# Optimization experiments

Measured on AMD Instinct MI355X. Metric: run time of the kernel, lower is better.

The kernel has to match this reference:

```python
import jax, jax.numpy as jnp
import numpy as np

B, S, D, H, HD = 1, 4096, 1024, 16, 64
HALF = HD // 2


def setup_inputs() -> dict:
    key = jax.random.key(0)
    ks = jax.random.split(key, 8)
    std = 0.02
    x = jax.random.normal(ks[0], (B, S, D), dtype=jnp.float32)
    wq_w = jax.random.normal(ks[1], (D, D), dtype=jnp.float32) * std
    wk_w = jax.random.normal(ks[2], (D, D), dtype=jnp.float32) * std
    wv_w = jax.random.normal(ks[3], (D, D), dtype=jnp.float32) * std
    wo_w = jax.random.normal(ks[4], (D, D), dtype=jnp.float32) * std
    wq_b = jnp.zeros((D,), jnp.float32)
    wk_b = jnp.zeros((D,), jnp.float32)
    wv_b = jnp.zeros((D,), jnp.float32)
    wo_b = jnp.zeros((D,), jnp.float32)
    # LLaMA-style rotary frequencies: theta = 10000^{-2i/HD}
    inv_freq = 1.0 / (10000.0 ** (jnp.arange(0, HD, 2, dtype=jnp.float32) / HD))  # [HALF]
    t = jnp.arange(S, dtype=jnp.float32)
    angles = jnp.outer(t, inv_freq)  # [S, HALF]
    freqs_cos = jnp.cos(angles)
    freqs_sin = jnp.sin(angles)
    # causal additive mask (finite large-negative to stay grad-safe)
    mask = jnp.triu(jnp.full((S, S), -1e9, dtype=jnp.float32), k=1)[None, None]
    return {
        "x": x, "start_pos": 0, "freqs_cos": freqs_cos, "freqs_sin": freqs_sin,
        "mask": mask,
        "wq_w": wq_w, "wq_b": wq_b, "wk_w": wk_w, "wk_b": wk_b,
        "wv_w": wv_w, "wv_b": wv_b, "wo_w": wo_w, "wo_b": wo_b,
    }


def _apply_rope(t, cos, sin):
    # t: [B, S, H, HD]; cos/sin: [S, HALF]. Complex multiply on consecutive pairs.
    b, s, h, hd = t.shape
    t2 = t.reshape(b, s, h, hd // 2, 2)
    x0, x1 = t2[..., 0], t2[..., 1]
    c = cos[None, :, None, :]
    sn = sin[None, :, None, :]
    o0 = x0 * c - x1 * sn
    o1 = x0 * sn + x1 * c
    return jnp.stack([o0, o1], axis=-1).reshape(b, s, h, hd)


def reference(x, start_pos, freqs_cos, freqs_sin, mask,
              wq_w, wq_b, wk_w, wk_b, wv_w, wv_b, wo_w, wo_b):
    bsz, seqlen, dim = x.shape
    q = (x @ wq_w.T + wq_b).reshape(bsz, seqlen, H, HD)
    k = (x @ wk_w.T + wk_b).reshape(bsz, seqlen, H, HD)
    v = (x @ wv_w.T + wv_b).reshape(bsz, seqlen, H, HD)
    q = _apply_rope(q, freqs_cos, freqs_sin)
    k = _apply_rope(k, freqs_cos, freqs_sin)
    # [B, H, S, HD]
    q = q.transpose(0, 2, 1, 3)
    k = k.transpose(0, 2, 1, 3)
    v = v.transpose(0, 2, 1, 3)
    scores = jnp.einsum('bhqd,bhkd->bhqk', q, k) / jnp.sqrt(jnp.float32(HD))
    scores = scores + mask
    probs = jax.nn.softmax(scores.astype(jnp.float32), axis=-1).astype(q.dtype)
    out = jnp.einsum('bhqk,bhkd->bhqd', probs, v)  # [B, H, S, HD]
    out = out.transpose(0, 2, 1, 3).reshape(bsz, seqlen, dim)
    return out @ wo_w.T + wo_b
```

## Files before the change

### kernel.cpp

```cpp
#include <hip/hip_runtime.h>


#define S_LEN 4096
#define DIM   1024
#define NH    16
#define HD    64

typedef __attribute__((ext_vector_type(8))) short bf16x8;
typedef __attribute__((ext_vector_type(4))) float f32x4;

__device__ __forceinline__ unsigned short f2b(float f) {
  union { float f; unsigned int u; } v; v.f = f;
  unsigned int r = (v.u + 0x7fffu + ((v.u >> 16) & 1u)) >> 16;
  return (unsigned short)r;
}
__device__ __forceinline__ float b2f(unsigned short h) {
  union { unsigned int u; float f; } v; v.u = ((unsigned int)h) << 16;
  return v.f;
}
__device__ __forceinline__ unsigned int pk2t(float a, float b) {
  union { float f; unsigned int u; } x, y; x.f = a; y.f = b;
  return (x.u >> 16) | (y.u & 0xffff0000u);
}
__device__ __forceinline__ void gload16(const void* g, void* l) {
  __builtin_amdgcn_global_load_lds(
      (const __attribute__((address_space(1))) unsigned int*)g,
      (__attribute__((address_space(3))) unsigned int*)l, 16, 0, 0);
}
__device__ __forceinline__ f32x4 fzero4() { f32x4 z = {0.f, 0.f, 0.f, 0.f}; return z; }

__global__ void cvt_all(const float* __restrict__ x, const float* __restrict__ wq,
                        const float* __restrict__ wk, const float* __restrict__ wv,
                        const float* __restrict__ wo, const float* __restrict__ qb,
                        const float* __restrict__ kb, const float* __restrict__ vbs,
                        const float* __restrict__ ob, unsigned short* __restrict__ xb,
                        unsigned short* __restrict__ wqkvb, unsigned short* __restrict__ wobb,
                        float* __restrict__ biasq, float* __restrict__ biaso) {
  int i = blockIdx.x * 256 + threadIdx.x;
  if (i < 2097152) {
    const float* src; unsigned short* dst; int off;
    if (i < 1048576)      { src = x;  dst = xb;              off = i; }
    else if (i < 1310720) { src = wq; dst = wqkvb;           off = i - 1048576; }
    else if (i < 1572864) { src = wk; dst = wqkvb + 1048576; off = i - 1310720; }
    else if (i < 1835008) { src = wv; dst = wqkvb + 2097152; off = i - 1572864; }
    else                  { src = wo; dst = wobb;            off = i - 1835008; }
    float4 v = ((const float4*)src)[off];
    unsigned int lo = (unsigned int)f2b(v.x) | ((unsigned int)f2b(v.y) << 16);
    unsigned int hi = (unsigned int)f2b(v.z) | ((unsigned int)f2b(v.w) << 16);
    ((uint2*)dst)[off] = make_uint2(lo, hi);
  } else if (i < 2097152 + 1024) {
    int j = i - 2097152;
    if (j < 256)      ((float4*)biasq)[j]              = ((const float4*)qb)[j];
    else if (j < 512) ((float4*)(biasq + 1024))[j-256] = ((const float4*)kb)[j-256];
    else if (j < 768) ((float4*)(biasq + 2048))[j-512] = ((const float4*)vbs)[j-512];
    else              ((float4*)biaso)[j-768]          = ((const float4*)ob)[j-768];
  }
}

__global__ __launch_bounds__(256) void gemm_qkv(
    const unsigned short* __restrict__ A, const unsigned short* __restrict__ B,
    const float* __restrict__ bias, unsigned short* __restrict__ dq,
    unsigned short* __restrict__ dk, unsigned short* __restrict__ vtout,
    const float* __restrict__ fc, const float* __restrict__ fs, int K) {
  __shared__ alignas(16) unsigned short sA[2][128 * 32];
  __shared__ alignas(16) unsigned short sB[2][128 * 32];
  const int tid = threadIdx.x;
  const int lane = tid & 63, wave = tid >> 6;
  const int ln = lane & 15, quad = lane >> 4;
  const int bm = blockIdx.x * 128, bn = blockIdx.y * 128;
  const int wr = (wave >> 1) * 64, wc = (wave & 1) * 64;

  f32x4 acc[4][4];
#pragma unroll
  for (int i = 0; i < 4; ++i)
#pragma unroll
    for (int j = 0; j < 4; ++j) acc[i][j] = fzero4();

#pragma unroll
  for (int i = 0; i < 2; ++i) {
    int o = (i * 256 + tid) * 16;
    int e = o >> 1;
    int row = e >> 5, col = e & 31;
    gload16(A + (size_t)(bm + row) * K + col, (char*)sA[0] + o);
    gload16(B + (size_t)(bn + row) * K + col, (char*)sB[0] + o);
  }

  int buf = 0;
  for (int k0 = 0; k0 < K; k0 += 32, buf ^= 1) {
    __syncthreads();
    if (k0 + 32 < K) {
#pragma unroll
      for (int i = 0; i < 2; ++i) {
        int o = (i * 256 + tid) * 16;
        int e = o >> 1;
        int row = e >> 5, col = e & 31;
        gload16(A + (size_t)(bm + row) * K + k0 + 32 + col, (char*)sA[buf ^ 1] + o);
        gload16(B + (size_t)(bn + row) * K + k0 + 32 + col, (char*)sB[buf ^ 1] + o);
      }
    }
    bf16x8 af[4], bfr[4];
#pragma unroll
    for (int i = 0; i < 4; ++i) {
      af[i]  = *(const bf16x8*)&sA[buf][(wr + i * 16 + ln) * 32 + quad * 8];
      bfr[i] = *(const bf16x8*)&sB[buf][(wc + i * 16 + ln) * 32 + quad * 8];
    }
#pragma unroll
    for (int i = 0; i < 4; ++i)
#pragma unroll
      for (int j = 0; j < 4; ++j)
        acc[i][j] = __builtin_amdgcn_mfma_f32_16x16x32_bf16(af[i], bfr[j], acc[i][j], 0, 0, 0);
  }

  const int bufi = bn >> 10;
  const int hq = ((bn & 1023) + wc) >> 6;
  if (bufi < 2) {
    unsigned short* const base = bufi == 0 ? dq : dk;
    const float qsc = bufi == 0 ? 0.180336880f : 1.0f;
#pragma unroll
    for (int i = 0; i < 4; ++i)
#pragma unroll
      for (int j = 0; j < 4; ++j) {
        int n = bn + wc + j * 16 + ln;
        float bi = bias[n];
        int hd = j * 16 + ln;
        int pi = hd >> 1;
        bool evn = (ln & 1) == 0;
#pragma unroll
        for (int r = 0; r < 4; ++r) {
          int m = bm + wr + i * 16 + quad * 4 + r;
          float val = acc[i][j][r] + bi;
          float par = __shfl_xor(val, 1);
          float c = fc[m * 32 + pi], sn = fs[m * 32 + pi];
          float o = evn ? (val * c - par * sn) : (par * sn + val * c);
          base[((size_t)(hq * S_LEN + m)) * HD + hd] = f2b(o * qsc);
        }
      }
  } else {
    __syncthreads();
    unsigned short* scr =
        (wave < 2 ? (unsigned short*)sA : (unsigned short*)sB) + (wave & 1) * 4096;
#pragma unroll
    for (int i = 0; i < 4; ++i)
#pragma unroll
      for (int j = 0; j < 4; ++j) {
        int n = bn + wc + j * 16 + ln;
        float bi = bias[n];
        int hd = j * 16 + ln;
#pragma unroll
        for (int r = 0; r < 4; ++r) {
          int sl = i * 16 + quad * 4 + r;
          int byte = hd * 128 + ((((sl >> 3) ^ (hd & 7)) << 4)) + (sl & 7) * 2;
          *(unsigned short*)((char*)scr + byte) = f2b(acc[i][j][r] + bi);
        }
      }
#pragma unroll
    for (int pass = 0; pass < 4; ++pass) {
      int row = pass * 16 + ln;
      uint4 d0 = *(uint4*)((char*)scr + row * 128 + (((quad * 2) ^ (row & 7)) << 4));
      uint4 d1 = *(uint4*)((char*)scr + row * 128 + (((quad * 2 + 1) ^ (row & 7)) << 4));
      uint4* dst = (uint4*)(vtout + ((size_t)(hq * HD + row)) * S_LEN + bm + wr + quad * 16);
      dst[0] = d0;
      dst[1] = d1;
    }
  }
}

__global__ __launch_bounds__(256) void gemm_out(
    const unsigned short* __restrict__ A, const unsigned short* __restrict__ B,
    const float* __restrict__ bias, float* __restrict__ outF, int N, int K) {
  __shared__ alignas(16) unsigned short sA[2][128 * 32];
  __shared__ alignas(16) unsigned short sB[2][64 * 32];
  const int tid = threadIdx.x;
  const int lane = tid & 63, wave = tid >> 6;
  const int ln = lane & 15, quad = lane >> 4;
  const int bm = blockIdx.x * 128, bn = blockIdx.y * 64;
  const int wr = (wave >> 1) * 64, wc = (wave & 1) * 32;

  f32x4 acc[4][2];
#pragma unroll
  for (int i = 0; i < 4; ++i)
#pragma unroll
    for (int j = 0; j < 2; ++j) acc[i][j] = fzero4();

  {
#pragma unroll
    for (int i = 0; i < 2; ++i) {
      int o = (i * 256 + tid) * 16;
      int e = o >> 1;
      int row = e >> 5, col = e & 31;
      gload16(A + (size_t)(bm + row) * K + col, (char*)sA[0] + o);
    }
    int o = tid * 16;
    int e = o >> 1;
    int row = e >> 5, col = e & 31;
    gload16(B + (size_t)(bn + row) * K + col, (char*)sB[0] + o);
  }

  int buf = 0;
  for (int k0 = 0; k0 < K; k0 += 32, buf ^= 1) {
    __syncthreads();
    if (k0 + 32 < K) {
#pragma unroll
      for (int i = 0; i < 2; ++i) {
        int o = (i * 256 + tid) * 16;
        int e = o >> 1;
        int row = e >> 5, col = e & 31;
        gload16(A + (size_t)(bm + row) * K + k0 + 32 + col, (char*)sA[buf ^ 1] + o);
      }
      int o = tid * 16;
      int e = o >> 1;
      int row = e >> 5, col = e & 31;
      gload16(B + (size_t)(bn + row) * K + k0 + 32 + col, (char*)sB[buf ^ 1] + o);
    }
    bf16x8 af[4], bfr[2];
#pragma unroll
    for (int i = 0; i < 4; ++i)
      af[i] = *(const bf16x8*)&sA[buf][(wr + i * 16 + ln) * 32 + quad * 8];
#pragma unroll
    for (int j = 0; j < 2; ++j)
      bfr[j] = *(const bf16x8*)&sB[buf][(wc + j * 16 + ln) * 32 + quad * 8];
#pragma unroll
    for (int i = 0; i < 4; ++i)
#pragma unroll
      for (int j = 0; j < 2; ++j)
        acc[i][j] = __builtin_amdgcn_mfma_f32_16x16x32_bf16(af[i], bfr[j], acc[i][j], 0, 0, 0);
  }

#pragma unroll
  for (int i = 0; i < 4; ++i)
#pragma unroll
    for (int j = 0; j < 2; ++j) {
      int n = bn + wc + j * 16 + ln;
      float bi = bias[n];
#pragma unroll
      for (int r = 0; r < 4; ++r) {
        int m = bm + wr + i * 16 + quad * 4 + r;
        outF[(size_t)m * N + n] = acc[i][j][r] + bi;
      }
    }
}

__device__ __forceinline__ bf16x8 lds_swzK(const unsigned short* s, int row, int chunk) {
  int byte = row * 128 + ((chunk ^ ((row >> 2) & 7)) << 4);
  return *(const bf16x8*)((const char*)s + byte);
}
__device__ __forceinline__ bf16x8 lds_swzV(const unsigned short* s, int row, int chunk) {
  int byte = row * 128 + ((chunk ^ (row & 7)) << 4);
  return *(const bf16x8*)((const char*)s + byte);
}

__global__ __launch_bounds__(256, 4) void flash_kernel(
    const unsigned short* __restrict__ qg, const unsigned short* __restrict__ kg,
    const unsigned short* __restrict__ vtg, unsigned short* __restrict__ attn) {
  __shared__ alignas(16) unsigned short sK[2][64 * 64];
  __shared__ alignas(16) unsigned short sV[2][64 * 64];
  __shared__ alignas(16) unsigned short sP[4 * 16 * 72];

  const int tid = threadIdx.x;
  const int lane = tid & 63, wave = tid >> 6;
  const int ln = lane & 15, quad = lane >> 4;
  const int c = blockIdx.x;
  const int h = 2 * (c & 7) + ((c >> 3) & 1);
  const int xp = c >> 4;

  const unsigned short* qh = qg + (size_t)h * (S_LEN * HD);
  const unsigned short* kh = kg + (size_t)h * (S_LEN * HD);
  const unsigned short* vh = vtg + (size_t)h * (HD * S_LEN);

  bf16x8 ones;
#pragma unroll
  for (int j = 0; j < 8; ++j) ones[j] = (short)0x3F80;
  unsigned short* pw = &sP[wave * (16 * 72)];

  for (int p = 0; p < 2; ++p) {
    const int qb = p == 0 ? xp : 63 - xp;
    const int q0 = qb * 64;
    const int qrow = q0 + wave * 16;

    bf16x8 qf[2];
    qf[0] = *(const bf16x8*)(qh + (size_t)(qrow + ln) * HD + quad * 8);
    qf[1] = *(const bf16x8*)(qh + (size_t)(qrow + ln) * HD + 32 + quad * 8);

    f32x4 o_acc[4];
    f32x4 l_acc = fzero4();
#pragma unroll
    for (int t = 0; t < 4; ++t) o_acc[t] = fzero4();

    const int nkv = qb + 1;

    __syncthreads();
#pragma unroll
    for (int i = 0; i < 2; ++i) {
      int ob = (i * 256 + tid) * 16;
      int row = ob >> 7;
      int ch = (ob >> 4) & 7;
      gload16(kh + (size_t)row * HD + ((ch ^ ((row >> 2) & 7)) << 3), (char*)sK[0] + ob);
      gload16(vh + (size_t)row * S_LEN + ((ch ^ (row & 7)) << 3), (char*)sV[0] + ob);
    }

    int buf = 0;
    for (int kt = 0; kt < nkv; ++kt, buf ^= 1) {
      const int kv0 = kt * 64;
      __syncthreads();
      if (kt + 1 < nkv) {
        const int kv1 = kv0 + 64;
#pragma unroll
        for (int i = 0; i < 2; ++i) {
          int ob = (i * 256 + tid) * 16;
          int row = ob >> 7;
          int ch = (ob >> 4) & 7;
          gload16(kh + (size_t)(kv1 + row) * HD + ((ch ^ ((row >> 2) & 7)) << 3),
                  (char*)sK[buf ^ 1] + ob);
          gload16(vh + (size_t)row * S_LEN + kv1 + ((ch ^ (row & 7)) << 3),
                  (char*)sV[buf ^ 1] + ob);
        }
      }

      const unsigned short* kp = sK[buf];
      const unsigned short* vp = sV[buf];
      f32x4 sc[4];
#pragma unroll
      for (int t = 0; t < 4; ++t) sc[t] = fzero4();
#pragma unroll
      for (int t = 0; t < 4; ++t) {
        int krow = ln * 4 + t;
        bf16x8 kb0 = lds_swzK(kp, krow, quad);
        bf16x8 kb1 = lds_swzK(kp, krow, 4 + quad);
        sc[t] = __builtin_amdgcn_mfma_f32_16x16x32_bf16(qf[0], kb0, sc[t], 0, 0, 0);
        sc[t] = __builtin_amdgcn_mfma_f32_16x16x32_bf16(qf[1], kb1, sc[t], 0, 0, 0);
      }

      if (kt == nkv - 1) {
#pragma unroll
        for (int r = 0; r < 4; ++r) {
          int row = qrow + quad * 4 + r;
          int colb = kv0 + ln * 4;
          float p0 = (colb + 0 <= row) ? __builtin_amdgcn_exp2f(sc[0][r]) : 0.0f;
          float p1 = (colb + 1 <= row) ? __builtin_amdgcn_exp2f(sc[1][r]) : 0.0f;
          float p2 = (colb + 2 <= row) ? __builtin_amdgcn_exp2f(sc[2][r]) : 0.0f;
          float p3 = (colb + 3 <= row) ? __builtin_amdgcn_exp2f(sc[3][r]) : 0.0f;
          *(uint2*)&pw[(quad * 4 + r) * 72 + ln * 4] = make_uint2(pk2t(p0, p1), pk2t(p2, p3));
        }
      } else {
#pragma unroll
        for (int r = 0; r < 4; ++r) {
          float p0 = __builtin_amdgcn_exp2f(sc[0][r]);
          float p1 = __builtin_amdgcn_exp2f(sc[1][r]);
          float p2 = __builtin_amdgcn_exp2f(sc[2][r]);
          float p3 = __builtin_amdgcn_exp2f(sc[3][r]);
          *(uint2*)&pw[(quad * 4 + r) * 72 + ln * 4] = make_uint2(pk2t(p0, p1), pk2t(p2, p3));
        }
      }

      bf16x8 pa0 = *(const bf16x8*)&pw[ln * 72 + quad * 8];
      bf16x8 pa1 = *(const bf16x8*)&pw[ln * 72 + 32 + quad * 8];

      l_acc = __builtin_amdgcn_mfma_f32_16x16x32_bf16(pa0, ones, l_acc, 0, 0, 0);
      l_acc = __builtin_amdgcn_mfma_f32_16x16x32_bf16(pa1, ones, l_acc, 0, 0, 0);

#pragma unroll
      for (int t = 0; t < 4; ++t) {
        int vrow = t * 16 + ln;
        bf16x8 vb0 = lds_swzV(vp, vrow, quad);
        bf16x8 vb1 = lds_swzV(vp, vrow, 4 + quad);
        o_acc[t] = __builtin_amdgcn_mfma_f32_16x16x32_bf16(pa0, vb0, o_acc[t], 0, 0, 0);
        o_acc[t] = __builtin_amdgcn_mfma_f32_16x16x32_bf16(pa1, vb1, o_acc[t], 0, 0, 0);
      }
    }

    float inv[4];
#pragma unroll
    for (int r = 0; r < 4; ++r) inv[r] = 1.0f / l_acc[r];
#pragma unroll
    for (int t = 0; t < 4; ++t)
#pragma unroll
      for (int r = 0; r < 4; ++r) {
        int row = qrow + quad * 4 + r;
        attn[(size_t)row * DIM + h * HD + t * 16 + ln] = f2b(o_acc[t][r] * inv[r]);
      }
  }
}

extern "C" void kernel_launch(void* const* d_in, const int* in_sizes, int n_in,
                              void* d_out, int out_size, void* d_ws, size_t ws_size,
                              hipStream_t stream) {
  const float* x    = (const float*)d_in[0];
  const float* fc   = (const float*)d_in[2];
  const float* fs   = (const float*)d_in[3];
  const float* wqw  = (const float*)d_in[5];
  const float* wqb  = (const float*)d_in[6];
  const float* wkw  = (const float*)d_in[7];
  const float* wkb  = (const float*)d_in[8];
  const float* wvw  = (const float*)d_in[9];
  const float* wvb  = (const float*)d_in[10];
  const float* wow  = (const float*)d_in[11];
  const float* wobf = (const float*)d_in[12];
  float* out = (float*)d_out;

  char* ws = (char*)d_ws;
  const size_t MB = (size_t)1 << 20;
  unsigned short* xb    = (unsigned short*)(ws + 0);
  unsigned short* wqkvb = (unsigned short*)(ws + 8 * MB);
  unsigned short* wobb  = (unsigned short*)(ws + 16 * MB);
  float* biasq = (float*)(ws + 18 * MB);
  float* biaso = (float*)(ws + 18 * MB + 65536);
  unsigned short* qb_ = (unsigned short*)(ws + 19 * MB);
  unsigned short* kb_ = (unsigned short*)(ws + 27 * MB);
  unsigned short* vt  = (unsigned short*)(ws + 35 * MB);
  unsigned short* attn = (unsigned short*)(ws + 0);

  cvt_all<<<8196, 256, 0, stream>>>(x, wqw, wkw, wvw, wow, wqb, wkb, wvb, wobf,
                                    xb, wqkvb, wobb, biasq, biaso);
  gemm_qkv<<<dim3(32, 24), 256, 0, stream>>>(xb, wqkvb, biasq, qb_, kb_, vt, fc, fs, 1024);
  flash_kernel<<<512, 256, 0, stream>>>(qb_, kb_, vt, attn);
  gemm_out<<<dim3(32, 16), 256, 0, stream>>>(attn, wobb, biaso, out, 1024, 1024);
}
```

Before: 267.7 us.

## Process paired causal query tiles concurrently in one 512-thread block sharing K/V loads

Each block now runs 8 waves, split into two groups that handle a short and a long causal query tile at the same time, instead of processing the two tiles one after the other. The groups share the double-buffered K/V tiles in LDS, which halves K/V global loads for the pair. The group whose tile is already complete skips compute via a continue but still takes part in loads and barriers. Block ordering is also remapped so heavier pairs are scheduled first. The cost is idle waves in the short-tile group during the tail of the loop.

```diff
diff --git a/kernel.cpp b/kernel.cpp
--- a/kernel.cpp
+++ b/kernel.cpp
@@ -249,136 +249,122 @@
   return *(const bf16x8*)((const char*)s + byte);
 }
 
-__global__ __launch_bounds__(256, 4) void flash_kernel(
+__global__ __launch_bounds__(512, 2) void flash_kernel(
     const unsigned short* __restrict__ qg, const unsigned short* __restrict__ kg,
     const unsigned short* __restrict__ vtg, unsigned short* __restrict__ attn) {
   __shared__ alignas(16) unsigned short sK[2][64 * 64];
   __shared__ alignas(16) unsigned short sV[2][64 * 64];
-  __shared__ alignas(16) unsigned short sP[4 * 16 * 72];
+  __shared__ alignas(16) unsigned short sP[8 * 16 * 72];
 
   const int tid = threadIdx.x;
   const int lane = tid & 63, wave = tid >> 6;
+  const int w = wave & 3, grp = wave >> 2;
   const int ln = lane & 15, quad = lane >> 4;
   const int c = blockIdx.x;
   const int h = 2 * (c & 7) + ((c >> 3) & 1);
-  const int xp = c >> 4;
+  const int u = c >> 4;
+  const int a = (u < 16) ? u : 47 - u;
+  const int q0 = (grp == 0 ? a : 63 - a) * 64;
+  const int qrow = q0 + w * 16;
 
   const unsigned short* qh = qg + (size_t)h * (S_LEN * HD);
   const unsigned short* kh = kg + (size_t)h * (S_LEN * HD);
   const unsigned short* vh = vtg + (size_t)h * (HD * S_LEN);
 
+  bf16x8 qf[2];
+  qf[0] = *(const bf16x8*)(qh + (size_t)(qrow + ln) * HD + quad * 8);
+  qf[1] = *(const bf16x8*)(qh + (size_t)(qrow + ln) * HD + 32 + quad * 8);
+
+  f32x4 o_acc[4];
+  f32x4 l_acc = fzero4();
+#pragma unroll
+  for (int t = 0; t < 4; ++t) o_acc[t] = fzero4();
   bf16x8 ones;
 #pragma unroll
   for (int j = 0; j < 8; ++j) ones[j] = (short)0x3F80;
   unsigned short* pw = &sP[wave * (16 * 72)];
 
-  for (int p = 0; p < 2; ++p) {
-    const int qb = p == 0 ? xp : 63 - xp;
-    const int q0 = qb * 64;
-    const int qrow = q0 + wave * 16;
-
-    bf16x8 qf[2];
-    qf[0] = *(const bf16x8*)(qh + (size_t)(qrow + ln) * HD + quad * 8);
-    qf[1] = *(const bf16x8*)(qh + (size_t)(qrow + ln) * HD + 32 + quad * 8);
-
-    f32x4 o_acc[4];
-    f32x4 l_acc = fzero4();
-#pragma unroll
-    for (int t = 0; t < 4; ++t) o_acc[t] = fzero4();
-
-    const int nkv = qb + 1;
-
+  const int nkv = 64 - a;
+  const int srow = tid >> 3, sch = tid & 7;
+
+  gload16(kh + (size_t)srow * HD + ((sch ^ ((srow >> 2) & 7)) << 3), (char*)sK[0] + tid * 16);
+  gload16(vh + (size_t)srow * S_LEN + ((sch ^ (srow & 7)) << 3), (char*)sV[0] + tid * 16);
+
+  int buf = 0;
+  for (int kt = 0; kt < nkv; ++kt, buf ^= 1) {
+    const int kv0 = kt * 64;
     __syncthreads();
-#pragma unroll
-    for (int i = 0; i < 2; ++i) {
-      int ob = (i * 256 + tid) * 16;
-      int row = ob >> 7;
-      int ch = (ob >> 4) & 7;
-      gload16(kh + (size_t)row * HD + ((ch ^ ((row >> 2) & 7)) << 3), (char*)sK[0] + ob);
-      gload16(vh + (size_t)row * S_LEN + ((ch ^ (row & 7)) << 3), (char*)sV[0] + ob);
-    }
-
-    int buf = 0;
-    for (int kt = 0; kt < nkv; ++kt, buf ^= 1) {
-      const int kv0 = kt * 64;
-      __syncthreads();
-      if (kt + 1 < nkv) {
-        const int kv1 = kv0 + 64;
-#pragma unroll
-        for (int i = 0; i < 2; ++i) {
-          int ob = (i * 256 + tid) * 16;
-          int row = ob >> 7;
-          int ch = (ob >> 4) & 7;
-          gload16(kh + (size_t)(kv1 + row) * HD + ((ch ^ ((row >> 2) & 7)) << 3),
-                  (char*)sK[buf ^ 1] + ob);
-          gload16(vh + (size_t)row * S_LEN + kv1 + ((ch ^ (row & 7)) << 3),
-                  (char*)sV[buf ^ 1] + ob);
-        }
-      }
-
-      const unsigned short* kp = sK[buf];
-      const unsigned short* vp = sV[buf];
-      f32x4 sc[4];
-#pragma unroll
-      for (int t = 0; t < 4; ++t) sc[t] = fzero4();
-#pragma unroll
-      for (int t = 0; t < 4; ++t) {
-        int krow = ln * 4 + t;
-        bf16x8 kb0 = lds_swzK(kp, krow, quad);
-        bf16x8 kb1 = lds_swzK(kp, krow, 4 + quad);
-        sc[t] = __builtin_amdgcn_mfma_f32_16x16x32_bf16(qf[0], kb0, sc[t], 0, 0, 0);
-        sc[t] = __builtin_amdgcn_mfma_f32_16x16x32_bf16(qf[1], kb1, sc[t], 0, 0, 0);
-      }
-
-      if (kt == nkv - 1) {
-#pragma unroll
-        for (int r = 0; r < 4; ++r) {
-          int row = qrow + quad * 4 + r;
-          int colb = kv0 + ln * 4;
-          float p0 = (colb + 0 <= row) ? __builtin_amdgcn_exp2f(sc[0][r]) : 0.0f;
-          float p1 = (colb + 1 <= row) ? __builtin_amdgcn_exp2f(sc[1][r]) : 0.0f;
-          float p2 = (colb + 2 <= row) ? __builtin_amdgcn_exp2f(sc[2][r]) : 0.0f;
-          float p3 = (colb + 3 <= row) ? __builtin_amdgcn_exp2f(sc[3][r]) : 0.0f;
-          *(uint2*)&pw[(quad * 4 + r) * 72 + ln * 4] = make_uint2(pk2t(p0, p1), pk2t(p2, p3));
-        }
-      } else {
-#pragma unroll
-        for (int r = 0; r < 4; ++r) {
-          float p0 = __builtin_amdgcn_exp2f(sc[0][r]);
-          float p1 = __builtin_amdgcn_exp2f(sc[1][r]);
-          float p2 = __builtin_amdgcn_exp2f(sc[2][r]);
-          float p3 = __builtin_amdgcn_exp2f(sc[3][r]);
-          *(uint2*)&pw[(quad * 4 + r) * 72 + ln * 4] = make_uint2(pk2t(p0, p1), pk2t(p2, p3));
-        }
-      }
-
-      bf16x8 pa0 = *(const bf16x8*)&pw[ln * 72 + quad * 8];
-      bf16x8 pa1 = *(const bf16x8*)&pw[ln * 72 + 32 + quad * 8];
-
-      l_acc = __builtin_amdgcn_mfma_f32_16x16x32_bf16(pa0, ones, l_acc, 0, 0, 0);
-      l_acc = __builtin_amdgcn_mfma_f32_16x16x32_bf16(pa1, ones, l_acc, 0, 0, 0);
-
-#pragma unroll
-      for (int t = 0; t < 4; ++t) {
-        int vrow = t * 16 + ln;
-        bf16x8 vb0 = lds_swzV(vp, vrow, quad);
-        bf16x8 vb1 = lds_swzV(vp, vrow, 4 + quad);
-        o_acc[t] = __builtin_amdgcn_mfma_f32_16x16x32_bf16(pa0, vb0, o_acc[t], 0, 0, 0);
-        o_acc[t] = __builtin_amdgcn_mfma_f32_16x16x32_bf16(pa1, vb1, o_acc[t], 0, 0, 0);
-      }
-    }
-
-    float inv[4];
-#pragma unroll
-    for (int r = 0; r < 4; ++r) inv[r] = 1.0f / l_acc[r];
-#pragma unroll
-    for (int t = 0; t < 4; ++t)
+    if (kt + 1 < nkv) {
+      const int kv1 = kv0 + 64;
+      gload16(kh + (size_t)(kv1 + srow) * HD + ((sch ^ ((srow >> 2) & 7)) << 3),
+              (char*)sK[buf ^ 1] + tid * 16);
+      gload16(vh + (size_t)srow * S_LEN + kv1 + ((sch ^ (srow & 7)) << 3),
+              (char*)sV[buf ^ 1] + tid * 16);
+    }
+    if (kv0 > qrow + 15) continue;
+
+    const unsigned short* kp = sK[buf];
+    const unsigned short* vp = sV[buf];
+    f32x4 sc[4];
+#pragma unroll
+    for (int t = 0; t < 4; ++t) sc[t] = fzero4();
+#pragma unroll
+    for (int t = 0; t < 4; ++t) {
+      int krow = ln * 4 + t;
+      bf16x8 kb0 = lds_swzK(kp, krow, quad);
+      bf16x8 kb1 = lds_swzK(kp, krow, 4 + quad);
+      sc[t] = __builtin_amdgcn_mfma_f32_16x16x32_bf16(qf[0], kb0, sc[t], 0, 0, 0);
+      sc[t] = __builtin_amdgcn_mfma_f32_16x16x32_bf16(qf[1], kb1, sc[t], 0, 0, 0);
+    }
+
+    if (kv0 == q0) {
 #pragma unroll
       for (int r = 0; r < 4; ++r) {
         int row = qrow + quad * 4 + r;
-        attn[(size_t)row * DIM + h * HD + t * 16 + ln] = f2b(o_acc[t][r] * inv[r]);
-      }
-  }
+        int colb = kv0 + ln * 4;
+        float p0 = (colb + 0 <= row) ? __builtin_amdgcn_exp2f(sc[0][r]) : 0.0f;
+        float p1 = (colb + 1 <= row) ? __builtin_amdgcn_exp2f(sc[1][r]) : 0.0f;
+        float p2 = (colb + 2 <= row) ? __builtin_amdgcn_exp2f(sc[2][r]) : 0.0f;
+        float p3 = (colb + 3 <= row) ? __builtin_amdgcn_exp2f(sc[3][r]) : 0.0f;
+        *(uint2*)&pw[(quad * 4 + r) * 72 + ln * 4] = make_uint2(pk2t(p0, p1), pk2t(p2, p3));
+      }
+    } else {
+#pragma unroll
+      for (int r = 0; r < 4; ++r) {
+        float p0 = __builtin_amdgcn_exp2f(sc[0][r]);
+        float p1 = __builtin_amdgcn_exp2f(sc[1][r]);
+        float p2 = __builtin_amdgcn_exp2f(sc[2][r]);
+        float p3 = __builtin_amdgcn_exp2f(sc[3][r]);
+        *(uint2*)&pw[(quad * 4 + r) * 72 + ln * 4] = make_uint2(pk2t(p0, p1), pk2t(p2, p3));
+      }
+    }
+
+    bf16x8 pa0 = *(const bf16x8*)&pw[ln * 72 + quad * 8];
+    bf16x8 pa1 = *(const bf16x8*)&pw[ln * 72 + 32 + quad * 8];
+
+    l_acc = __builtin_amdgcn_mfma_f32_16x16x32_bf16(pa0, ones, l_acc, 0, 0, 0);
+    l_acc = __builtin_amdgcn_mfma_f32_16x16x32_bf16(pa1, ones, l_acc, 0, 0, 0);
+
+#pragma unroll
+    for (int t = 0; t < 4; ++t) {
+      int vrow = t * 16 + ln;
+      bf16x8 vb0 = lds_swzV(vp, vrow, quad);
+      bf16x8 vb1 = lds_swzV(vp, vrow, 4 + quad);
+      o_acc[t] = __builtin_amdgcn_mfma_f32_16x16x32_bf16(pa0, vb0, o_acc[t], 0, 0, 0);
+      o_acc[t] = __builtin_amdgcn_mfma_f32_16x16x32_bf16(pa1, vb1, o_acc[t], 0, 0, 0);
+    }
+  }
+
+  float inv[4];
+#pragma unroll
+  for (int r = 0; r < 4; ++r) inv[r] = 1.0f / l_acc[r];
+#pragma unroll
+  for (int t = 0; t < 4; ++t)
+#pragma unroll
+    for (int r = 0; r < 4; ++r) {
+      int row = qrow + quad * 4 + r;
+      attn[(size_t)row * DIM + h * HD + t * 16 + ln] = f2b(o_acc[t][r] * inv[r]);
+    }
 }
 
 extern "C" void kernel_launch(void* const* d_in, const int* in_sizes, int n_in,
@@ -412,6 +398,6 @@
   cvt_all<<<8196, 256, 0, stream>>>(x, wqw, wkw, wvw, wow, wqb, wkb, wvb, wobf,
                                     xb, wqkvb, wobb, biasq, biaso);
   gemm_qkv<<<dim3(32, 24), 256, 0, stream>>>(xb, wqkvb, biasq, qb_, kb_, vt, fc, fs, 1024);
-  flash_kernel<<<512, 256, 0, stream>>>(qb_, kb_, vt, attn);
+  flash_kernel<<<512, 512, 0, stream>>>(qb_, kb_, vt, attn);
   gemm_out<<<dim3(32, 16), 256, 0, stream>>>(attn, wobb, biaso, out, 1024, 1024);
 }
```

Result: no change. 267.4 us (-0.1%).
